# Optimization experiments

Hardware: AMD Instinct MI355X
Metric: run time of the kernel (lower is better)

## Reference

```python
import jax, jax.numpy as jnp
import numpy as np

B, L, H, N = 8, 2048, 512, 64  # batch, seq_len, d_model, SSM state size


def setup_inputs() -> dict:
    key = jax.random.key(0)
    ks = jax.random.split(key, 10)
    x = jax.random.normal(ks[0], (B, L, H), jnp.float32)
    # S4D-style parameters (diagonal SSM, S4D-Lin init)
    log_dt = jnp.log(1e-3) + jax.random.uniform(ks[1], (H,), jnp.float32) * (jnp.log(1e-1) - jnp.log(1e-3))
    A_re = -0.5 * jnp.ones((H, N), jnp.float32)
    A_im = jnp.tile(np.pi * jnp.arange(N, dtype=np.float32), (H, 1))
    C_re = jax.random.normal(ks[2], (H, N), jnp.float32) * (0.5 ** 0.5)
    C_im = jax.random.normal(ks[3], (H, N), jnp.float32) * (0.5 ** 0.5)
    D_skip = jax.random.normal(ks[4], (H,), jnp.float32)
    # S4 output linear (GLU): d_model -> 2*d_model, then gated
    W_out = jax.random.normal(ks[5], (2 * H, H), jnp.float32) / np.sqrt(H)
    b_out = jnp.zeros((2 * H,), jnp.float32)
    # LayerNorms
    g1 = jnp.ones((H,), jnp.float32); beta1 = jnp.zeros((H,), jnp.float32)
    g2 = jnp.ones((H,), jnp.float32); beta2 = jnp.zeros((H,), jnp.float32)
    # 1x1 conv FFN (kernel_size=1 => pointwise linear), d_ff = d_model
    W1 = jax.random.normal(ks[6], (H, H), jnp.float32) / np.sqrt(H)
    bc1 = jnp.zeros((H,), jnp.float32)
    W2 = jax.random.normal(ks[7], (H, H), jnp.float32) / np.sqrt(H)
    bc2 = jnp.zeros((H,), jnp.float32)
    return dict(x=x, log_dt=log_dt, A_re=A_re, A_im=A_im, C_re=C_re, C_im=C_im,
                D_skip=D_skip, W_out=W_out, b_out=b_out, g1=g1, beta1=beta1,
                g2=g2, beta2=beta2, W1=W1, bc1=bc1, W2=W2, bc2=bc2)


def _layer_norm(x, g, b):
    mu = jnp.mean(x, axis=-1, keepdims=True)
    var = jnp.mean((x - mu) ** 2, axis=-1, keepdims=True)
    return (x - mu) / jnp.sqrt(var + 1e-5) * g + b


def _s4(x, log_dt, A_re, A_im, C_re, C_im, D_skip, W_out, b_out):
    # x: (B, L, H) channels-last (transposed=False)
    Lx = x.shape[1]
    dt = jnp.exp(log_dt)                       # (H,)
    A = A_re + 1j * A_im                       # (H, N) diagonal state matrix
    dtA = A * dt[:, None]
    # ZOH discretization of C: Ct = C * (exp(dt*A) - 1) / A
    Ct = (C_re + 1j * C_im) * ((jnp.exp(dtA) - 1.0) / A)
    # Vandermonde kernel: K[h, l] = 2 Re sum_n Ct[h,n] exp(dt*A[h,n]*l)
    l = jnp.arange(Lx, dtype=jnp.float32)
    K = 2.0 * jnp.real(jnp.einsum('hn,hnl->hl', Ct, jnp.exp(dtA[:, :, None] * l)))
    # FFT long convolution (linear conv via zero-padded circular conv)
    u = jnp.swapaxes(x, 1, 2)                  # (B, H, L)
    n = 2 * Lx
    y = jnp.fft.irfft(jnp.fft.rfft(u, n) * jnp.fft.rfft(K, n)[None], n)[..., :Lx]
    y = y + D_skip[None, :, None] * u          # skip connection D*u
    y = jax.nn.gelu(y)                         # S4 default activation
    # output linear + GLU (S4 default postact)
    z = jnp.einsum('bhl,fh->bfl', y, W_out) + b_out[None, :, None]
    a, g = jnp.split(z, 2, axis=1)
    y = a * jax.nn.sigmoid(g)
    return jnp.swapaxes(y, 1, 2)               # (B, L, H)


def reference(x, log_dt, A_re, A_im, C_re, C_im, D_skip, W_out, b_out,
              g1, beta1, g2, beta2, W1, bc1, W2, bc2):
    new_x = _s4(x, log_dt, A_re, A_im, C_re, C_im, D_skip, W_out, b_out)
    x = x + new_x
    x = _layer_norm(x, g1, beta1)
    # FFN via 1x1 convs (pointwise linears); dropout is identity in eval
    y = jax.nn.relu(jnp.einsum('blh,fh->blf', x, W1) + bc1)
    y = jnp.einsum('blf,hf->blh', y, W2) + bc2
    return _layer_norm(x + y, g2, beta2)
```

## Files before the change

### kernel.cpp

```cpp
#include <hip/hip_runtime.h>
#include <cstddef>
#include <cstdint>

#define B_DIM 8
#define L_DIM 2048
#define H_DIM 512
#define N_DIM 64
#define HN (H_DIM * N_DIM)
#define BLH (B_DIM * L_DIM * H_DIM)
#define M_DIM (B_DIM * L_DIM)

typedef unsigned short u16;
typedef short bf16x8 __attribute__((ext_vector_type(8)));
typedef float floatx4 __attribute__((ext_vector_type(4)));

__device__ __forceinline__ float sigmoidf_(float v) {
    return 1.0f / (1.0f + __expf(-v));
}

__device__ __forceinline__ float gelu_tanh_(float x) {
    float x3 = x * x * x;
    float z = 0.7978845608028654f * fmaf(0.044715f, x3, x);
    float e = __expf(-2.0f * fabsf(z));
    float th = (1.0f - e) / (1.0f + e);
    th = copysignf(th, z);
    return 0.5f * x * (1.0f + th);
}

__device__ __forceinline__ u16 f2b(float f) {
    unsigned u = __float_as_uint(f);
    unsigned r = (u + 0x7fffu + ((u >> 16) & 1u)) >> 16;
    return (u16)r;
}
__device__ __forceinline__ float b2f(u16 u) {
    return __uint_as_float(((unsigned)u) << 16);
}
__device__ __forceinline__ void unpack2(unsigned u, float& a, float& b) {
    a = __uint_as_float(u << 16);
    b = __uint_as_float(u & 0xffff0000u);
}
__device__ __forceinline__ unsigned pack2(float a, float b) {
    return (unsigned)f2b(a) | ((unsigned)f2b(b) << 16);
}

__device__ __forceinline__ void csq(float& r, float& i) {
    float nr = r * r - i * i;
    i = 2.0f * r * i;
    r = nr;
}

__global__ __launch_bounds__(256) void cast3_kernel(
    const float* __restrict__ s0, const float* __restrict__ s1,
    const float* __restrict__ s2, u16* __restrict__ d0,
    u16* __restrict__ d1, u16* __restrict__ d2)
{
    int bid = blockIdx.x;
    const float* src; u16* dst; int off;
    if (bid < 512)      { src = s0; dst = d0; off = bid; }
    else if (bid < 768) { src = s1; dst = d1; off = bid - 512; }
    else                { src = s2; dst = d2; off = bid - 768; }
    int i = off * 256 + threadIdx.x;
    float4 v = *(const float4*)(src + (size_t)i * 4);
    uint2 p;
    p.x = pack2(v.x, v.y);
    p.y = pack2(v.z, v.w);
    *(uint2*)(dst + (size_t)i * 4) = p;
}

__global__ __launch_bounds__(256) void params_kernel(
    const float* __restrict__ log_dt, const float* __restrict__ A_re,
    const float* __restrict__ A_im, const float* __restrict__ C_re,
    const float* __restrict__ C_im, float* __restrict__ P,
    u16* __restrict__ Toep_bf)
{
    __shared__ float ktab_s[4][64];
    const int t = threadIdx.x;
    const int wv = t >> 6, lane = t & 63;
    const int i = blockIdx.x * 256 + t;
    const int h = i >> 6;

    float dt = expf(log_dt[h]);
    float Ar = A_re[i], Ai = A_im[i];
    float ar = dt * Ar, ai = dt * Ai;
    float e = expf(ar);
    float wr = e * cosf(ai);
    float wi = e * sinf(ai);
    float em1r = wr - 1.0f, em1i = wi;
    float inv = 1.0f / fmaf(Ar, Ar, Ai * Ai);
    float qr = fmaf(em1r, Ar, em1i * Ai) * inv;
    float qi = fmaf(em1i, Ar, -(em1r * Ai)) * inv;
    float Cr = C_re[i], Ci = C_im[i];
    float c2r = 2.0f * (Cr * qr - Ci * qi);
    float c2i = 2.0f * (Cr * qi + Ci * qr);
    P[i]          = wr;
    P[HN + i]     = wi;
    P[2 * HN + i] = c2r;
    P[3 * HN + i] = c2i;

    float pr = 1.0f, pi = 0.0f;
    for (int tau = 0; tau < 64; ++tau) {
        float term = c2r * pr - c2i * pi;
        #pragma unroll
        for (int m = 32; m > 0; m >>= 1) term += __shfl_xor(term, m, 64);
        if (lane == 0) ktab_s[wv][tau] = term;
        float nr = pr * wr - pi * wi, ni = pr * wi + pi * wr;
        pr = nr; pi = ni;
    }
    __syncthreads();

    const int h0 = blockIdx.x * 4;
    #pragma unroll
    for (int r = 0; r < 8; ++r) {
        int c = t + r * 256;
        int hh = c >> 9, rem = c & 511;
        int tt = rem >> 3, j0 = (rem & 7) * 8;
        u16 vv[8];
        #pragma unroll
        for (int jj = 0; jj < 8; ++jj) {
            int j = j0 + jj;
            vv[jj] = (j <= tt) ? f2b(ktab_s[hh][tt - j]) : (u16)0;
        }
        *(uint4*)&Toep_bf[((size_t)(h0 + hh) << 12) + (tt << 6) + j0] = *(uint4*)vv;
    }
}

__global__ __launch_bounds__(256) void xtrans_kernel(
    const float* __restrict__ x, u16* __restrict__ XT)
{
    __shared__ float tile[32][33];
    int b  = blockIdx.z;
    int l0 = blockIdx.x * 32;
    int h0 = blockIdx.y * 32;
    int tx = threadIdx.x & 31;
    int ty = threadIdx.x >> 5;
    #pragma unroll
    for (int r = 0; r < 4; ++r)
        tile[ty + r * 8][tx] = x[((size_t)b * L_DIM + l0 + ty + r * 8) * H_DIM + h0 + tx];
    __syncthreads();
    #pragma unroll
    for (int r = 0; r < 4; ++r)
        XT[((size_t)b * H_DIM + h0 + ty + r * 8) * L_DIM + l0 + tx] = f2b(tile[tx][ty + r * 8]);
}

__global__ __launch_bounds__(256) void ssm_chunk_kernel(
    const u16* __restrict__ XT, const float* __restrict__ P,
    const u16* __restrict__ Toep_bf, const float* __restrict__ D_skip,
    u16* __restrict__ YT)
{
    __shared__ u16 U[128 * 72];
    __shared__ u16 S[128 * 136];
    __shared__ u16 EVT[13312];
    u16* E  = EVT;
    u16* Tp = EVT;
    u16* V  = EVT + 4608;

    const int h    = blockIdx.x;
    const int b0   = blockIdx.y * 4;
    const int t    = threadIdx.x;
    const int lane = t & 63;
    const int wv   = t >> 6;
    const int lm   = lane & 15, lq = lane >> 4;

    const int pidx = (h << 6) + lane;
    const float wr  = P[pidx],          wi  = P[HN + pidx];
    const float c2r = P[2 * HN + pidx], c2i = P[3 * HN + pidx];

    #pragma unroll
    for (int r = 0; r < 4; ++r) {
        int idx = t + r * 256;
        int row = idx >> 3, ch = idx & 7;
        const u16* gp = XT + (((size_t)(b0 + (row >> 5)) * H_DIM + h) << 11)
                           + ((row & 31) << 6) + (ch << 3);
        *(uint4*)&U[row * 72 + ch * 8] = *(const uint4*)gp;
    }

    float bwr, bwi;
    {
        float g16r = wr, g16i = wi;
        csq(g16r, g16i); csq(g16r, g16i); csq(g16r, g16i); csq(g16r, g16i);
        if (wv == 0)      { bwr = 1.0f; bwi = 0.0f; }
        else if (wv == 1) { bwr = g16r; bwi = g16i; }
        else if (wv == 2) { bwr = g16r; bwi = g16i; csq(bwr, bwi); }
        else {
            float g32r = g16r, g32i = g16i; csq(g32r, g32i);
            bwr = g32r * g16r - g32i * g16i;
            bwi = g32r * g16i + g32i * g16r;
        }
    }

    {
        float pr = bwr, pi = bwi;
        #pragma unroll
        for (int jk = 0; jk < 16; ++jk) {
            int k = (wv << 4) + jk;
            int j = 63 - k;
            E[(2 * lane) * 72 + j]     = f2b(pr);
            E[(2 * lane + 1) * 72 + j] = f2b(pi);
            float nr = pr * wr - pi * wi, ni = pr * wi + pi * wr;
            pr = nr; pi = ni;
        }
    }
    __syncthreads();

    {
        const int wm = wv >> 1, wn = wv & 1;
        floatx4 acc[4][4] = {};
        #pragma unroll
        for (int ks = 0; ks < 2; ++ks) {
            bf16x8 af[4], bfv[4];
            #pragma unroll
            for (int i = 0; i < 4; ++i)
                af[i] = *(const bf16x8*)&E[(wm * 64 + i * 16 + lm) * 72 + ks * 32 + lq * 8];
            #pragma unroll
            for (int j = 0; j < 4; ++j)
                bfv[j] = *(const bf16x8*)&U[(wn * 64 + j * 16 + lm) * 72 + ks * 32 + lq * 8];
            #pragma unroll
            for (int i = 0; i < 4; ++i) {
                #pragma unroll
                for (int j = 0; j < 4; ++j)
                    acc[i][j] = __builtin_amdgcn_mfma_f32_16x16x32_bf16(af[i], bfv[j], acc[i][j], 0, 0, 0);
            }
        }
        #pragma unroll
        for (int i = 0; i < 4; ++i) {
            #pragma unroll
            for (int j = 0; j < 4; ++j) {
                int ncol = wn * 64 + j * 16 + lm;
                int m0   = wm * 64 + i * 16 + lq * 4;
                u16 pk[4];
                #pragma unroll
                for (int r = 0; r < 4; ++r) pk[r] = f2b(acc[i][j][r]);
                *(uint2*)&S[ncol * 136 + m0] = *(uint2*)pk;
            }
        }
    }
    __syncthreads();

    {
        float pr = bwr, pi = bwi;
        {
            float nr = pr * wr - pi * wi, ni = pr * wi + pi * wr;
            pr = nr; pi = ni;
        }
        #pragma unroll
        for (int jk = 1; jk <= 16; ++jk) {
            int tr = (wv << 4) + jk - 1;
            float qr = c2r * pr - c2i * pi;
            float qi = c2r * pi + c2i * pr;
            V[tr * 136 + 2 * lane]     = f2b(qr);
            V[tr * 136 + 2 * lane + 1] = f2b(-qi);
            float nr = pr * wr - pi * wi, ni = pr * wi + pi * wr;
            pr = nr; pi = ni;
        }
        #pragma unroll
        for (int r = 0; r < 2; ++r) {
            int idx = t + r * 256;
            int row = idx >> 3, ch = idx & 7;
            *(uint4*)&Tp[row * 72 + ch * 8] =
                *(const uint4*)&Toep_bf[((size_t)h << 12) + (row << 6) + (ch << 3)];
        }
        float wTr = wr, wTi = wi;
        csq(wTr, wTi); csq(wTr, wTi); csq(wTr, wTi);
        csq(wTr, wTi); csq(wTr, wTi); csq(wTr, wTi);
        float Sr = 0.0f, Si = 0.0f;
        const int n2 = lane * 2;
        for (int c = 0; c < 32; ++c) {
            int base = (wv * 32 + c) * 136 + n2;
            unsigned lv = *(unsigned*)&S[base];
            float lr, li;
            unpack2(lv, lr, li);
            *(unsigned*)&S[base] = pack2(Sr, Si);
            float nSr = wTr * Sr - wTi * Si + lr;
            Si = wTr * Si + wTi * Sr + li;
            Sr = nSr;
        }
    }
    __syncthreads();

    {
        const float Dh = D_skip[h];
        floatx4 acc[4][2] = {};
        #pragma unroll
        for (int ks = 0; ks < 6; ++ks) {
            bf16x8 af[4], bfv[2];
            if (ks < 2) {
                #pragma unroll
                for (int i = 0; i < 4; ++i)
                    af[i] = *(const bf16x8*)&Tp[(i * 16 + lm) * 72 + ks * 32 + lq * 8];
                #pragma unroll
                for (int j = 0; j < 2; ++j)
                    bfv[j] = *(const bf16x8*)&U[(wv * 32 + j * 16 + lm) * 72 + ks * 32 + lq * 8];
            } else {
                #pragma unroll
                for (int i = 0; i < 4; ++i)
                    af[i] = *(const bf16x8*)&V[(i * 16 + lm) * 136 + (ks - 2) * 32 + lq * 8];
                #pragma unroll
                for (int j = 0; j < 2; ++j)
                    bfv[j] = *(const bf16x8*)&S[(wv * 32 + j * 16 + lm) * 136 + (ks - 2) * 32 + lq * 8];
            }
            #pragma unroll
            for (int i = 0; i < 4; ++i) {
                #pragma unroll
                for (int j = 0; j < 2; ++j)
                    acc[i][j] = __builtin_amdgcn_mfma_f32_16x16x32_bf16(af[i], bfv[j], acc[i][j], 0, 0, 0);
            }
        }
        #pragma unroll
        for (int j = 0; j < 2; ++j) {
            int ncol = wv * 32 + j * 16 + lm;
            int bloc = ncol >> 5, c = ncol & 31;
            size_t gbase = (((size_t)(b0 + bloc) * H_DIM + h) << 11) + (c << 6);
            #pragma unroll
            for (int i = 0; i < 4; ++i) {
                int t0 = i * 16 + lq * 4;
                u16 upk[4];
                *(uint2*)upk = *(const uint2*)&U[ncol * 72 + t0];
                u16 opk[4];
                #pragma unroll
                for (int r = 0; r < 4; ++r) {
                    float uvv = b2f(upk[r]);
                    float yv = gelu_tanh_(fmaf(Dh, uvv, acc[i][j][r]));
                    opk[r] = f2b(yv);
                }
                *(uint2*)&YT[gbase + t0] = *(uint2*)opk;
            }
        }
    }
}

__global__ __launch_bounds__(256) void ytrans_kernel(
    const u16* __restrict__ YT, u16* __restrict__ Y)
{
    __shared__ u16 tile[32][33];
    int b  = blockIdx.z;
    int l0 = blockIdx.x * 32;
    int h0 = blockIdx.y * 32;
    int tx = threadIdx.x & 31;
    int ty = threadIdx.x >> 5;
    #pragma unroll
    for (int r = 0; r < 4; ++r)
        tile[ty + r * 8][tx] = YT[((size_t)b * H_DIM + h0 + ty + r * 8) * L_DIM + l0 + tx];
    __syncthreads();
    #pragma unroll
    for (int r = 0; r < 4; ++r)
        Y[((size_t)b * L_DIM + l0 + ty + r * 8) * H_DIM + h0 + tx] = tile[tx][ty + r * 8];
}

__device__ __forceinline__ void stage_tile_512(
    const u16* __restrict__ g, u16* lds, int row0, int k0)
{
    const int t = threadIdx.x;
    const int row  = t >> 2;
    const int csrc = (t & 3) ^ ((t >> 3) & 3);
    const u16* gp = g + (size_t)(row0 + row) * 512 + k0 + csrc * 8;
    __builtin_amdgcn_global_load_lds(
        (const __attribute__((address_space(1))) unsigned int*)gp,
        (__attribute__((address_space(3))) unsigned int*)(lds + (size_t)t * 8),
        16, 0, 0);
}

__global__ __launch_bounds__(512) void gemm1_glu_kernel(
    const u16* __restrict__ A, const u16* __restrict__ Wo,
    const float* __restrict__ bo, const float* __restrict__ x,
    u16* __restrict__ out)
{
    __shared__ u16 As[2][128 * 32];
    __shared__ u16 Ba[2][128 * 32];
    __shared__ u16 Bg[2][128 * 32];
    const int t    = threadIdx.x;
    const int lane = t & 63;
    const int wv   = t >> 6;
    const int wm   = wv >> 2, wn = wv & 3;
    const int lm   = lane & 15, lq = lane >> 4;
    const int sw   = (lq ^ ((lm >> 1) & 3)) * 8;
    const int m0   = blockIdx.x * 128, n0 = blockIdx.y * 128;
    floatx4 accA[4][2] = {};
    floatx4 accG[4][2] = {};

    stage_tile_512(A, As[0], m0, 0);
    stage_tile_512(Wo, Ba[0], n0, 0);
    stage_tile_512(Wo, Bg[0], 512 + n0, 0);
    __syncthreads();

    int cur = 0;
    for (int k0 = 32; k0 < 512; k0 += 32) {
        const int nx = cur ^ 1;
        stage_tile_512(A, As[nx], m0, k0);
        stage_tile_512(Wo, Ba[nx], n0, k0);
        stage_tile_512(Wo, Bg[nx], 512 + n0, k0);

        bf16x8 af[4], ba[2], bg[2];
        #pragma unroll
        for (int i = 0; i < 4; ++i)
            af[i] = *(const bf16x8*)&As[cur][(wm * 64 + i * 16 + lm) * 32 + sw];
        #pragma unroll
        for (int j = 0; j < 2; ++j) {
            ba[j] = *(const bf16x8*)&Ba[cur][(wn * 32 + j * 16 + lm) * 32 + sw];
            bg[j] = *(const bf16x8*)&Bg[cur][(wn * 32 + j * 16 + lm) * 32 + sw];
        }
        #pragma unroll
        for (int i = 0; i < 4; ++i) {
            #pragma unroll
            for (int j = 0; j < 2; ++j) {
                accA[i][j] = __builtin_amdgcn_mfma_f32_16x16x32_bf16(af[i], ba[j], accA[i][j], 0, 0, 0);
                accG[i][j] = __builtin_amdgcn_mfma_f32_16x16x32_bf16(af[i], bg[j], accG[i][j], 0, 0, 0);
            }
        }
        __syncthreads();
        cur = nx;
    }
    {
        bf16x8 af[4], ba[2], bg[2];
        #pragma unroll
        for (int i = 0; i < 4; ++i)
            af[i] = *(const bf16x8*)&As[cur][(wm * 64 + i * 16 + lm) * 32 + sw];
        #pragma unroll
        for (int j = 0; j < 2; ++j) {
            ba[j] = *(const bf16x8*)&Ba[cur][(wn * 32 + j * 16 + lm) * 32 + sw];
            bg[j] = *(const bf16x8*)&Bg[cur][(wn * 32 + j * 16 + lm) * 32 + sw];
        }
        #pragma unroll
        for (int i = 0; i < 4; ++i) {
            #pragma unroll
            for (int j = 0; j < 2; ++j) {
                accA[i][j] = __builtin_amdgcn_mfma_f32_16x16x32_bf16(af[i], ba[j], accA[i][j], 0, 0, 0);
                accG[i][j] = __builtin_amdgcn_mfma_f32_16x16x32_bf16(af[i], bg[j], accG[i][j], 0, 0, 0);
            }
        }
    }
    #pragma unroll
    for (int j = 0; j < 2; ++j) {
        int n = n0 + wn * 32 + j * 16 + lm;
        float bav = bo[n], bgv = bo[512 + n];
        #pragma unroll
        for (int i = 0; i < 4; ++i) {
            #pragma unroll
            for (int r = 0; r < 4; ++r) {
                int m = m0 + wm * 64 + i * 16 + lq * 4 + r;
                float av = accA[i][j][r] + bav;
                float gv = accG[i][j][r] + bgv;
                float xv = x[(size_t)m * 512 + n];
                out[(size_t)m * 512 + n] = f2b(fmaf(av, sigmoidf_(gv), xv));
            }
        }
    }
}

__global__ __launch_bounds__(512) void gemm_relu_kernel(
    const u16* __restrict__ A, const u16* __restrict__ Bw,
    const float* __restrict__ bias, u16* __restrict__ C)
{
    __shared__ u16 As[2][128 * 32];
    __shared__ u16 Bs[2][128 * 32];
    const int t    = threadIdx.x;
    const int lane = t & 63;
    const int wv   = t >> 6;
    const int wm   = wv >> 2, wn = wv & 3;
    const int lm   = lane & 15, lq = lane >> 4;
    const int sw   = (lq ^ ((lm >> 1) & 3)) * 8;
    const int m0   = blockIdx.x * 128, n0 = blockIdx.y * 128;
    floatx4 acc[4][2] = {};

    stage_tile_512(A, As[0], m0, 0);
    stage_tile_512(Bw, Bs[0], n0, 0);
    __syncthreads();

    int cur = 0;
    for (int k0 = 32; k0 < 512; k0 += 32) {
        const int nx = cur ^ 1;
        stage_tile_512(A, As[nx], m0, k0);
        stage_tile_512(Bw, Bs[nx], n0, k0);

        bf16x8 af[4], bfr[2];
        #pragma unroll
        for (int i = 0; i < 4; ++i)
            af[i] = *(const bf16x8*)&As[cur][(wm * 64 + i * 16 + lm) * 32 + sw];
        #pragma unroll
        for (int j = 0; j < 2; ++j)
            bfr[j] = *(const bf16x8*)&Bs[cur][(wn * 32 + j * 16 + lm) * 32 + sw];
        #pragma unroll
        for (int i = 0; i < 4; ++i) {
            #pragma unroll
            for (int j = 0; j < 2; ++j)
                acc[i][j] = __builtin_amdgcn_mfma_f32_16x16x32_bf16(af[i], bfr[j], acc[i][j], 0, 0, 0);
        }
        __syncthreads();
        cur = nx;
    }
    {
        bf16x8 af[4], bfr[2];
        #pragma unroll
        for (int i = 0; i < 4; ++i)
            af[i] = *(const bf16x8*)&As[cur][(wm * 64 + i * 16 + lm) * 32 + sw];
        #pragma unroll
        for (int j = 0; j < 2; ++j)
            bfr[j] = *(const bf16x8*)&Bs[cur][(wn * 32 + j * 16 + lm) * 32 + sw];
        #pragma unroll
        for (int i = 0; i < 4; ++i) {
            #pragma unroll
            for (int j = 0; j < 2; ++j)
                acc[i][j] = __builtin_amdgcn_mfma_f32_16x16x32_bf16(af[i], bfr[j], acc[i][j], 0, 0, 0);
        }
    }
    #pragma unroll
    for (int j = 0; j < 2; ++j) {
        int n = n0 + wn * 32 + j * 16 + lm;
        float bv = bias[n];
        #pragma unroll
        for (int i = 0; i < 4; ++i) {
            #pragma unroll
            for (int r = 0; r < 4; ++r) {
                int m = m0 + wm * 64 + i * 16 + lq * 4 + r;
                float v = fmaxf(acc[i][j][r] + bv, 0.0f);
                C[(size_t)m * 512 + n] = f2b(v);
            }
        }
    }
}

__global__ __launch_bounds__(512) void gemm2_ln_kernel(
    const u16* __restrict__ A, const u16* __restrict__ Bw,
    const float* __restrict__ bias, const u16* __restrict__ res,
    const float* __restrict__ gamma, const float* __restrict__ beta,
    float* __restrict__ out)
{
    __shared__ u16 As[2][32 * 32];
    __shared__ u16 Bs[2][512 * 32];
    __shared__ float2 lnred[32 * 8];
    const int t    = threadIdx.x;
    const int lane = t & 63;
    const int wv   = t >> 6;
    const int lm   = lane & 15, lq = lane >> 4;
    const int sw   = (lq ^ ((lm >> 1) & 3)) * 8;
    const int m0   = blockIdx.x * 32;
    floatx4 acc[2][4] = {};

    const int csrc = (t & 3) ^ ((t >> 3) & 3);

    {
        #pragma unroll
        for (int r = 0; r < 4; ++r) {
            int row = (t >> 2) + r * 128;
            const u16* gp = Bw + (size_t)row * 512 + csrc * 8;
            __builtin_amdgcn_global_load_lds(
                (const __attribute__((address_space(1))) unsigned int*)gp,
                (__attribute__((address_space(3))) unsigned int*)(&Bs[0][0] + (size_t)t * 8 + (size_t)r * 4096),
                16, 0, 0);
        }
        if (t < 128) {
            int row = t >> 2;
            const u16* gp = A + (size_t)(m0 + row) * 512 + csrc * 8;
            __builtin_amdgcn_global_load_lds(
                (const __attribute__((address_space(1))) unsigned int*)gp,
                (__attribute__((address_space(3))) unsigned int*)(&As[0][0] + (size_t)t * 8),
                16, 0, 0);
        }
    }
    __syncthreads();

    int cur = 0;
    for (int k0 = 32; k0 < 512; k0 += 32) {
        const int nx = cur ^ 1;
        #pragma unroll
        for (int r = 0; r < 4; ++r) {
            int row = (t >> 2) + r * 128;
            const u16* gp = Bw + (size_t)row * 512 + k0 + csrc * 8;
            __builtin_amdgcn_global_load_lds(
                (const __attribute__((address_space(1))) unsigned int*)gp,
                (__attribute__((address_space(3))) unsigned int*)(&Bs[nx][0] + (size_t)t * 8 + (size_t)r * 4096),
                16, 0, 0);
        }
        if (t < 128) {
            int row = t >> 2;
            const u16* gp = A + (size_t)(m0 + row) * 512 + k0 + csrc * 8;
            __builtin_amdgcn_global_load_lds(
                (const __attribute__((address_space(1))) unsigned int*)gp,
                (__attribute__((address_space(3))) unsigned int*)(&As[nx][0] + (size_t)t * 8),
                16, 0, 0);
        }

        bf16x8 af[2], bfr[4];
        #pragma unroll
        for (int i = 0; i < 2; ++i)
            af[i] = *(const bf16x8*)&As[cur][(i * 16 + lm) * 32 + sw];
        #pragma unroll
        for (int j = 0; j < 4; ++j)
            bfr[j] = *(const bf16x8*)&Bs[cur][(wv * 64 + j * 16 + lm) * 32 + sw];
        #pragma unroll
        for (int i = 0; i < 2; ++i) {
            #pragma unroll
            for (int j = 0; j < 4; ++j)
                acc[i][j] = __builtin_amdgcn_mfma_f32_16x16x32_bf16(af[i], bfr[j], acc[i][j], 0, 0, 0);
        }
        __syncthreads();
        cur = nx;
    }
    {
        bf16x8 af[2], bfr[4];
        #pragma unroll
        for (int i = 0; i < 2; ++i)
            af[i] = *(const bf16x8*)&As[cur][(i * 16 + lm) * 32 + sw];
        #pragma unroll
        for (int j = 0; j < 4; ++j)
            bfr[j] = *(const bf16x8*)&Bs[cur][(wv * 64 + j * 16 + lm) * 32 + sw];
        #pragma unroll
        for (int i = 0; i < 2; ++i) {
            #pragma unroll
            for (int j = 0; j < 4; ++j)
                acc[i][j] = __builtin_amdgcn_mfma_f32_16x16x32_bf16(af[i], bfr[j], acc[i][j], 0, 0, 0);
        }
    }

    float bv[4], gv[4], btv[4];
    #pragma unroll
    for (int j = 0; j < 4; ++j) {
        int n = wv * 64 + j * 16 + lm;
        bv[j]  = bias[n];
        gv[j]  = gamma[n];
        btv[j] = beta[n];
    }
    #pragma unroll
    for (int i = 0; i < 2; ++i) {
        #pragma unroll
        for (int j = 0; j < 4; ++j) {
            int n = wv * 64 + j * 16 + lm;
            #pragma unroll
            for (int r = 0; r < 4; ++r) {
                int m = m0 + i * 16 + lq * 4 + r;
                acc[i][j][r] += bv[j] + b2f(res[(size_t)m * 512 + n]);
            }
        }
    }
    #pragma unroll
    for (int i = 0; i < 2; ++i) {
        #pragma unroll
        for (int r = 0; r < 4; ++r) {
            float s  = acc[i][0][r] + acc[i][1][r] + acc[i][2][r] + acc[i][3][r];
            float sq = acc[i][0][r] * acc[i][0][r] + acc[i][1][r] * acc[i][1][r]
                     + acc[i][2][r] * acc[i][2][r] + acc[i][3][r] * acc[i][3][r];
            #pragma unroll
            for (int msk = 1; msk < 16; msk <<= 1) {
                s  += __shfl_xor(s, msk, 64);
                sq += __shfl_xor(sq, msk, 64);
            }
            if (lm == 0) {
                float2 p; p.x = s; p.y = sq;
                lnred[(i * 16 + lq * 4 + r) * 8 + wv] = p;
            }
        }
    }
    __syncthreads();
    #pragma unroll
    for (int i = 0; i < 2; ++i) {
        #pragma unroll
        for (int r = 0; r < 4; ++r) {
            int row = i * 16 + lq * 4 + r;
            float s = 0.0f, sq = 0.0f;
            #pragma unroll
            for (int w = 0; w < 8; ++w) {
                float2 p = lnred[row * 8 + w];
                s += p.x; sq += p.y;
            }
            float mu  = s * (1.0f / 512.0f);
            float var = sq * (1.0f / 512.0f) - mu * mu;
            float rs  = rsqrtf(var + 1e-5f);
            #pragma unroll
            for (int j = 0; j < 4; ++j) {
                int n = wv * 64 + j * 16 + lm;
                out[(size_t)(m0 + row) * 512 + n] = fmaf((acc[i][j][r] - mu) * rs, gv[j], btv[j]);
            }
        }
    }
}

__global__ __launch_bounds__(256) void ln_bf_kernel(
    const u16* __restrict__ in,
    const float* __restrict__ gamma, const float* __restrict__ beta,
    u16* __restrict__ outb)
{
    int w    = threadIdx.x >> 6;
    int lane = threadIdx.x & 63;
    size_t row  = (size_t)blockIdx.x * 4 + w;
    size_t base = row * 512 + lane * 8;
    uint4 raw = *(const uint4*)(in + base);
    float v[8];
    unpack2(raw.x, v[0], v[1]); unpack2(raw.y, v[2], v[3]);
    unpack2(raw.z, v[4], v[5]); unpack2(raw.w, v[6], v[7]);
    float s = 0.0f, sq = 0.0f;
    #pragma unroll
    for (int i = 0; i < 8; ++i) { s += v[i]; sq = fmaf(v[i], v[i], sq); }
    #pragma unroll
    for (int m = 32; m > 0; m >>= 1) {
        s  += __shfl_xor(s, m, 64);
        sq += __shfl_xor(sq, m, 64);
    }
    float mu  = s * (1.0f / 512.0f);
    float var = sq * (1.0f / 512.0f) - mu * mu;
    float rs  = rsqrtf(var + 1e-5f);
    float g[8], bt[8];
    *(float4*)&g[0]  = *(const float4*)(gamma + lane * 8);
    *(float4*)&g[4]  = *(const float4*)(gamma + lane * 8 + 4);
    *(float4*)&bt[0] = *(const float4*)(beta + lane * 8);
    *(float4*)&bt[4] = *(const float4*)(beta + lane * 8 + 4);
    float o[8];
    #pragma unroll
    for (int i = 0; i < 8; ++i)
        o[i] = fmaf((v[i] - mu) * rs, g[i], bt[i]);
    uint4 p;
    p.x = pack2(o[0], o[1]); p.y = pack2(o[2], o[3]);
    p.z = pack2(o[4], o[5]); p.w = pack2(o[6], o[7]);
    *(uint4*)(outb + base) = p;
}

extern "C" void kernel_launch(void* const* d_in, const int* in_sizes, int n_in,
                              void* d_out, int out_size, void* d_ws, size_t ws_size,
                              hipStream_t stream)
{
    (void)in_sizes; (void)n_in; (void)out_size; (void)ws_size;
    const float* x      = (const float*)d_in[0];
    const float* log_dt = (const float*)d_in[1];
    const float* A_re   = (const float*)d_in[2];
    const float* A_im   = (const float*)d_in[3];
    const float* C_re   = (const float*)d_in[4];
    const float* C_im   = (const float*)d_in[5];
    const float* D_skip = (const float*)d_in[6];
    const float* W_out  = (const float*)d_in[7];
    const float* b_out  = (const float*)d_in[8];
    const float* g1     = (const float*)d_in[9];
    const float* beta1  = (const float*)d_in[10];
    const float* g2     = (const float*)d_in[11];
    const float* beta2  = (const float*)d_in[12];
    const float* W1     = (const float*)d_in[13];
    const float* bc1    = (const float*)d_in[14];
    const float* W2     = (const float*)d_in[15];
    const float* bc2    = (const float*)d_in[16];
    float* out = (float*)d_out;

    char*  wsb    = (char*)d_ws;
    float* P      = (float*)wsb;
    u16*   Toep   = (u16*)(wsb + 4 * HN * 4 + 512 * 64 * 4);
    u16*   Wobf   = Toep + 512 * 4096;
    u16*   W1bf   = Wobf + 1024 * 512;
    u16*   W2bf   = W1bf + 512 * 512;
    u16*   r1     = W2bf + 512 * 512;
    u16*   r2     = r1 + BLH;
    u16*   r3     = r2 + BLH;

    cast3_kernel<<<1024, 256, 0, stream>>>(W_out, W1, W2, Wobf, W1bf, W2bf);
    params_kernel<<<128, 256, 0, stream>>>(log_dt, A_re, A_im, C_re, C_im, P, Toep);
    xtrans_kernel<<<dim3(L_DIM / 32, H_DIM / 32, B_DIM), 256, 0, stream>>>(x, r1);
    ssm_chunk_kernel<<<dim3(H_DIM, 2), 256, 0, stream>>>(r1, P, Toep, D_skip, r2);
    ytrans_kernel<<<dim3(L_DIM / 32, H_DIM / 32, B_DIM), 256, 0, stream>>>(r2, r3);
    gemm1_glu_kernel<<<dim3(M_DIM / 128, 4), 512, 0, stream>>>(r3, Wobf, b_out, x, r2);
    ln_bf_kernel<<<M_DIM / 4, 256, 0, stream>>>(r2, g1, beta1, r1);
    gemm_relu_kernel<<<dim3(M_DIM / 128, 4), 512, 0, stream>>>(r1, W1bf, bc1, r3);
    gemm2_ln_kernel<<<M_DIM / 32, 512, 0, stream>>>(r3, W2bf, bc2, r1, g2, beta2, out);
}
```

Before: 245.1 us.

## Fold LayerNorm1 into GEMM epilogues, fuse y-transpose into GEMM1, merge setup kernels

Merges the weight casts, parameter/Toeplitz setup and x transpose into a single setup kernel. The y transpose is dropped: GEMM1 reads the transposed SSM output directly and transposes it while staging into LDS. The standalone LayerNorm1 is also removed. GEMM1 emits per-row partial sum and sum-of-squares, and GEMM-relu applies the normalization algebraically, using W1 pre-scaled by g1 plus precomputed W1·g1 and W1·beta1 vectors. The final kernel recomputes LN1 on the fly for its residual. This cuts launches and two full-tensor passes, at the cost of uncoalesced 8-element scattered LDS writes in GEMM1 and LN applied to bf16-quantized pre-norm activations.

Result: faster. 240.1 us (-2.0%).

```diff
diff --git a/kernel.cpp b/kernel.cpp
--- a/kernel.cpp
+++ b/kernel.cpp
@@ -49,97 +49,124 @@
     r = nr;
 }
 
-__global__ __launch_bounds__(256) void cast3_kernel(
-    const float* __restrict__ s0, const float* __restrict__ s1,
-    const float* __restrict__ s2, u16* __restrict__ d0,
-    u16* __restrict__ d1, u16* __restrict__ d2)
-{
-    int bid = blockIdx.x;
-    const float* src; u16* dst; int off;
-    if (bid < 512)      { src = s0; dst = d0; off = bid; }
-    else if (bid < 768) { src = s1; dst = d1; off = bid - 512; }
-    else                { src = s2; dst = d2; off = bid - 768; }
-    int i = off * 256 + threadIdx.x;
-    float4 v = *(const float4*)(src + (size_t)i * 4);
-    uint2 p;
-    p.x = pack2(v.x, v.y);
-    p.y = pack2(v.z, v.w);
-    *(uint2*)(dst + (size_t)i * 4) = p;
-}
-
-__global__ __launch_bounds__(256) void params_kernel(
+__global__ __launch_bounds__(256) void setup_kernel(
+    const float* __restrict__ x, const float* __restrict__ W_out,
+    const float* __restrict__ W1, const float* __restrict__ W2,
     const float* __restrict__ log_dt, const float* __restrict__ A_re,
     const float* __restrict__ A_im, const float* __restrict__ C_re,
-    const float* __restrict__ C_im, float* __restrict__ P,
-    u16* __restrict__ Toep_bf)
-{
-    __shared__ float ktab_s[4][64];
-    const int t = threadIdx.x;
-    const int wv = t >> 6, lane = t & 63;
-    const int i = blockIdx.x * 256 + t;
-    const int h = i >> 6;
-
-    float dt = expf(log_dt[h]);
-    float Ar = A_re[i], Ai = A_im[i];
-    float ar = dt * Ar, ai = dt * Ai;
-    float e = expf(ar);
-    float wr = e * cosf(ai);
-    float wi = e * sinf(ai);
-    float em1r = wr - 1.0f, em1i = wi;
-    float inv = 1.0f / fmaf(Ar, Ar, Ai * Ai);
-    float qr = fmaf(em1r, Ar, em1i * Ai) * inv;
-    float qi = fmaf(em1i, Ar, -(em1r * Ai)) * inv;
-    float Cr = C_re[i], Ci = C_im[i];
-    float c2r = 2.0f * (Cr * qr - Ci * qi);
-    float c2i = 2.0f * (Cr * qi + Ci * qr);
-    P[i]          = wr;
-    P[HN + i]     = wi;
-    P[2 * HN + i] = c2r;
-    P[3 * HN + i] = c2i;
-
-    float pr = 1.0f, pi = 0.0f;
-    for (int tau = 0; tau < 64; ++tau) {
-        float term = c2r * pr - c2i * pi;
-        #pragma unroll
-        for (int m = 32; m > 0; m >>= 1) term += __shfl_xor(term, m, 64);
-        if (lane == 0) ktab_s[wv][tau] = term;
-        float nr = pr * wr - pi * wi, ni = pr * wi + pi * wr;
-        pr = nr; pi = ni;
-    }
-    __syncthreads();
-
-    const int h0 = blockIdx.x * 4;
-    #pragma unroll
-    for (int r = 0; r < 8; ++r) {
-        int c = t + r * 256;
-        int hh = c >> 9, rem = c & 511;
-        int tt = rem >> 3, j0 = (rem & 7) * 8;
-        u16 vv[8];
-        #pragma unroll
-        for (int jj = 0; jj < 8; ++jj) {
-            int j = j0 + jj;
-            vv[jj] = (j <= tt) ? f2b(ktab_s[hh][tt - j]) : (u16)0;
-        }
-        *(uint4*)&Toep_bf[((size_t)(h0 + hh) << 12) + (tt << 6) + j0] = *(uint4*)vv;
-    }
-}
-
-__global__ __launch_bounds__(256) void xtrans_kernel(
-    const float* __restrict__ x, u16* __restrict__ XT)
+    const float* __restrict__ C_im, const float* __restrict__ g1,
+    const float* __restrict__ beta1,
+    u16* __restrict__ XT, u16* __restrict__ Wobf, u16* __restrict__ W1gbf,
+    u16* __restrict__ W2bf, float* __restrict__ P, u16* __restrict__ Toep_bf,
+    float* __restrict__ c1, float* __restrict__ c2)
 {
     __shared__ float tile[32][33];
-    int b  = blockIdx.z;
-    int l0 = blockIdx.x * 32;
-    int h0 = blockIdx.y * 32;
-    int tx = threadIdx.x & 31;
-    int ty = threadIdx.x >> 5;
-    #pragma unroll
-    for (int r = 0; r < 4; ++r)
-        tile[ty + r * 8][tx] = x[((size_t)b * L_DIM + l0 + ty + r * 8) * H_DIM + h0 + tx];
-    __syncthreads();
-    #pragma unroll
-    for (int r = 0; r < 4; ++r)
-        XT[((size_t)b * H_DIM + h0 + ty + r * 8) * L_DIM + l0 + tx] = f2b(tile[tx][ty + r * 8]);
+    __shared__ float ktab_s[4][64];
+    const int bid = blockIdx.x;
+    const int t   = threadIdx.x;
+
+    if (bid < 8192) {
+        int b  = bid >> 10;
+        int hy = (bid >> 6) & 15;
+        int lx = bid & 63;
+        int l0 = lx * 32, h0 = hy * 32;
+        int tx = t & 31, ty = t >> 5;
+        #pragma unroll
+        for (int r = 0; r < 4; ++r)
+            tile[ty + r * 8][tx] = x[((size_t)b * L_DIM + l0 + ty + r * 8) * H_DIM + h0 + tx];
+        __syncthreads();
+        #pragma unroll
+        for (int r = 0; r < 4; ++r)
+            XT[(((size_t)b * H_DIM + h0 + ty + r * 8) << 11) + l0 + tx] = f2b(tile[tx][ty + r * 8]);
+    } else if (bid < 9216) {
+        int off = bid - 8192;
+        if (off < 512) {
+            int i = off * 256 + t;
+            float4 v = *(const float4*)(W_out + (size_t)i * 4);
+            uint2 p; p.x = pack2(v.x, v.y); p.y = pack2(v.z, v.w);
+            *(uint2*)(Wobf + (size_t)i * 4) = p;
+        } else if (off < 768) {
+            int i = (off - 512) * 256 + t;
+            float4 v = *(const float4*)(W1 + (size_t)i * 4);
+            int n = (i * 4) & 511;
+            float4 g = *(const float4*)(g1 + n);
+            uint2 p; p.x = pack2(v.x * g.x, v.y * g.y);
+            p.y = pack2(v.z * g.z, v.w * g.w);
+            *(uint2*)(W1gbf + (size_t)i * 4) = p;
+        } else {
+            int i = (off - 768) * 256 + t;
+            float4 v = *(const float4*)(W2 + (size_t)i * 4);
+            uint2 p; p.x = pack2(v.x, v.y); p.y = pack2(v.z, v.w);
+            *(uint2*)(W2bf + (size_t)i * 4) = p;
+        }
+    } else if (bid < 9344) {
+        const int wv = t >> 6, lane = t & 63;
+        const int i = (bid - 9216) * 256 + t;
+        const int h = i >> 6;
+        float dt = expf(log_dt[h]);
+        float Ar = A_re[i], Ai = A_im[i];
+        float ar = dt * Ar, ai = dt * Ai;
+        float e = expf(ar);
+        float wr = e * cosf(ai);
+        float wi = e * sinf(ai);
+        float em1r = wr - 1.0f, em1i = wi;
+        float inv = 1.0f / fmaf(Ar, Ar, Ai * Ai);
+        float qr = fmaf(em1r, Ar, em1i * Ai) * inv;
+        float qi = fmaf(em1i, Ar, -(em1r * Ai)) * inv;
+        float Cr = C_re[i], Ci = C_im[i];
+        float c2r = 2.0f * (Cr * qr - Ci * qi);
+        float c2i = 2.0f * (Cr * qi + Ci * qr);
+        P[i]          = wr;
+        P[HN + i]     = wi;
+        P[2 * HN + i] = c2r;
+        P[3 * HN + i] = c2i;
+
+        float pr = 1.0f, pi = 0.0f;
+        for (int tau = 0; tau < 64; ++tau) {
+            float term = c2r * pr - c2i * pi;
+            #pragma unroll
+            for (int m = 32; m > 0; m >>= 1) term += __shfl_xor(term, m, 64);
+            if (lane == 0) ktab_s[wv][tau] = term;
+            float nr = pr * wr - pi * wi, ni = pr * wi + pi * wr;
+            pr = nr; pi = ni;
+        }
+        __syncthreads();
+
+        const int h0 = (bid - 9216) * 4;
+        #pragma unroll
+        for (int r = 0; r < 8; ++r) {
+            int c = t + r * 256;
+            int hh = c >> 9, rem = c & 511;
+            int tt = rem >> 3, j0 = (rem & 7) * 8;
+            u16 vv[8];
+            #pragma unroll
+            for (int jj = 0; jj < 8; ++jj) {
+                int j = j0 + jj;
+                vv[jj] = (j <= tt) ? f2b(ktab_s[hh][tt - j]) : (u16)0;
+            }
+            *(uint4*)&Toep_bf[((size_t)(h0 + hh) << 12) + (tt << 6) + j0] = *(uint4*)vv;
+        }
+    } else {
+        int f = (bid - 9344) * 4 + (t >> 6);
+        int lane = t & 63;
+        int n = lane * 8;
+        float4 w0 = *(const float4*)(W1 + (size_t)f * 512 + n);
+        float4 w1v = *(const float4*)(W1 + (size_t)f * 512 + n + 4);
+        float4 ga = *(const float4*)(g1 + n);
+        float4 gb = *(const float4*)(g1 + n + 4);
+        float4 b0 = *(const float4*)(beta1 + n);
+        float4 b1 = *(const float4*)(beta1 + n + 4);
+        float s1 = w0.x * ga.x + w0.y * ga.y + w0.z * ga.z + w0.w * ga.w
+                 + w1v.x * gb.x + w1v.y * gb.y + w1v.z * gb.z + w1v.w * gb.w;
+        float s2 = w0.x * b0.x + w0.y * b0.y + w0.z * b0.z + w0.w * b0.w
+                 + w1v.x * b1.x + w1v.y * b1.y + w1v.z * b1.z + w1v.w * b1.w;
+        #pragma unroll
+        for (int m = 32; m > 0; m >>= 1) {
+            s1 += __shfl_xor(s1, m, 64);
+            s2 += __shfl_xor(s2, m, 64);
+        }
+        if (lane == 0) { c1[f] = s1; c2[f] = s2; }
+    }
 }
 
 __global__ __launch_bounds__(256) void ssm_chunk_kernel(
@@ -328,24 +355,6 @@
     }
 }
 
-__global__ __launch_bounds__(256) void ytrans_kernel(
-    const u16* __restrict__ YT, u16* __restrict__ Y)
-{
-    __shared__ u16 tile[32][33];
-    int b  = blockIdx.z;
-    int l0 = blockIdx.x * 32;
-    int h0 = blockIdx.y * 32;
-    int tx = threadIdx.x & 31;
-    int ty = threadIdx.x >> 5;
-    #pragma unroll
-    for (int r = 0; r < 4; ++r)
-        tile[ty + r * 8][tx] = YT[((size_t)b * H_DIM + h0 + ty + r * 8) * L_DIM + l0 + tx];
-    __syncthreads();
-    #pragma unroll
-    for (int r = 0; r < 4; ++r)
-        Y[((size_t)b * L_DIM + l0 + ty + r * 8) * H_DIM + h0 + tx] = tile[tx][ty + r * 8];
-}
-
 __device__ __forceinline__ void stage_tile_512(
     const u16* __restrict__ g, u16* lds, int row0, int k0)
 {
@@ -359,14 +368,32 @@
         16, 0, 0);
 }
 
+__device__ __forceinline__ uint4 ldA_yt(
+    const u16* __restrict__ YT, int b, int l0, int k0)
+{
+    const int k  = threadIdx.x >> 4;
+    const int lc = threadIdx.x & 15;
+    return *(const uint4*)(YT + (((size_t)(b * 512 + k0 + k)) << 11) + l0 + lc * 8);
+}
+__device__ __forceinline__ void dswA(u16* lds, uint4 av)
+{
+    const int k  = threadIdx.x >> 4;
+    const int lc = threadIdx.x & 15;
+    u16* p = lds + (lc * 8) * 32 + (((k >> 3) ^ (lc & 3)) << 3) + (k & 7);
+    const u16* s = (const u16*)&av;
+    #pragma unroll
+    for (int j = 0; j < 8; ++j) p[j * 32] = s[j];
+}
+
 __global__ __launch_bounds__(512) void gemm1_glu_kernel(
-    const u16* __restrict__ A, const u16* __restrict__ Wo,
+    const u16* __restrict__ YT, const u16* __restrict__ Wo,
     const float* __restrict__ bo, const float* __restrict__ x,
-    u16* __restrict__ out)
+    u16* __restrict__ out, float2* __restrict__ Pstats)
 {
     __shared__ u16 As[2][128 * 32];
     __shared__ u16 Ba[2][128 * 32];
     __shared__ u16 Bg[2][128 * 32];
+    __shared__ float2 red1[128][4];
     const int t    = threadIdx.x;
     const int lane = t & 63;
     const int wv   = t >> 6;
@@ -374,25 +401,33 @@
     const int lm   = lane & 15, lq = lane >> 4;
     const int sw   = (lq ^ ((lm >> 1) & 3)) * 8;
     const int m0   = blockIdx.x * 128, n0 = blockIdx.y * 128;
+    const int b    = m0 >> 11;
+    const int l0   = m0 & 2047;
     floatx4 accA[4][2] = {};
     floatx4 accG[4][2] = {};
 
-    stage_tile_512(A, As[0], m0, 0);
+    int swA[4];
+    #pragma unroll
+    for (int i = 0; i < 4; ++i)
+        swA[i] = (lq ^ ((i * 2 + (lm >> 3)) & 3)) * 8;
+
+    uint4 av = ldA_yt(YT, b, l0, 0);
     stage_tile_512(Wo, Ba[0], n0, 0);
     stage_tile_512(Wo, Bg[0], 512 + n0, 0);
+    dswA(As[0], av);
     __syncthreads();
 
     int cur = 0;
     for (int k0 = 32; k0 < 512; k0 += 32) {
         const int nx = cur ^ 1;
-        stage_tile_512(A, As[nx], m0, k0);
+        uint4 avn = ldA_yt(YT, b, l0, k0);
         stage_tile_512(Wo, Ba[nx], n0, k0);
         stage_tile_512(Wo, Bg[nx], 512 + n0, k0);
 
         bf16x8 af[4], ba[2], bg[2];
         #pragma unroll
         for (int i = 0; i < 4; ++i)
-            af[i] = *(const bf16x8*)&As[cur][(wm * 64 + i * 16 + lm) * 32 + sw];
+            af[i] = *(const bf16x8*)&As[cur][(wm * 64 + i * 16 + lm) * 32 + swA[i]];
         #pragma unroll
         for (int j = 0; j < 2; ++j) {
             ba[j] = *(const bf16x8*)&Ba[cur][(wn * 32 + j * 16 + lm) * 32 + sw];
@@ -406,6 +441,7 @@
                 accG[i][j] = __builtin_amdgcn_mfma_f32_16x16x32_bf16(af[i], bg[j], accG[i][j], 0, 0, 0);
             }
         }
+        dswA(As[nx], avn);
         __syncthreads();
         cur = nx;
     }
@@ -413,7 +449,7 @@
         bf16x8 af[4], ba[2], bg[2];
         #pragma unroll
         for (int i = 0; i < 4; ++i)
-            af[i] = *(const bf16x8*)&As[cur][(wm * 64 + i * 16 + lm) * 32 + sw];
+            af[i] = *(const bf16x8*)&As[cur][(wm * 64 + i * 16 + lm) * 32 + swA[i]];
         #pragma unroll
         for (int j = 0; j < 2; ++j) {
             ba[j] = *(const bf16x8*)&Ba[cur][(wn * 32 + j * 16 + lm) * 32 + sw];
@@ -428,30 +464,57 @@
             }
         }
     }
+
+    float bav[2], bgv[2];
     #pragma unroll
     for (int j = 0; j < 2; ++j) {
         int n = n0 + wn * 32 + j * 16 + lm;
-        float bav = bo[n], bgv = bo[512 + n];
-        #pragma unroll
-        for (int i = 0; i < 4; ++i) {
-            #pragma unroll
-            for (int r = 0; r < 4; ++r) {
-                int m = m0 + wm * 64 + i * 16 + lq * 4 + r;
-                float av = accA[i][j][r] + bav;
-                float gv = accG[i][j][r] + bgv;
+        bav[j] = bo[n]; bgv[j] = bo[512 + n];
+    }
+    #pragma unroll
+    for (int i = 0; i < 4; ++i) {
+        #pragma unroll
+        for (int r = 0; r < 4; ++r) {
+            int row = wm * 64 + i * 16 + lq * 4 + r;
+            int m = m0 + row;
+            float s = 0.0f, sq = 0.0f;
+            #pragma unroll
+            for (int j = 0; j < 2; ++j) {
+                int n = n0 + wn * 32 + j * 16 + lm;
+                float a_ = accA[i][j][r] + bav[j];
+                float g_ = accG[i][j][r] + bgv[j];
                 float xv = x[(size_t)m * 512 + n];
-                out[(size_t)m * 512 + n] = f2b(fmaf(av, sigmoidf_(gv), xv));
-            }
-        }
+                float ov = fmaf(a_, sigmoidf_(g_), xv);
+                out[(size_t)m * 512 + n] = f2b(ov);
+                s += ov; sq = fmaf(ov, ov, sq);
+            }
+            #pragma unroll
+            for (int msk = 1; msk < 16; msk <<= 1) {
+                s  += __shfl_xor(s, msk, 64);
+                sq += __shfl_xor(sq, msk, 64);
+            }
+            if (lm == 0) { float2 p; p.x = s; p.y = sq; red1[row][wn] = p; }
+        }
+    }
+    __syncthreads();
+    if (t < 128) {
+        float s = 0.0f, sq = 0.0f;
+        #pragma unroll
+        for (int w = 0; w < 4; ++w) { float2 p = red1[t][w]; s += p.x; sq += p.y; }
+        float2 o; o.x = s; o.y = sq;
+        Pstats[(size_t)(m0 + t) * 4 + blockIdx.y] = o;
     }
 }
 
 __global__ __launch_bounds__(512) void gemm_relu_kernel(
     const u16* __restrict__ A, const u16* __restrict__ Bw,
-    const float* __restrict__ bias, u16* __restrict__ C)
+    const float* __restrict__ bias, const float2* __restrict__ Pstats,
+    const float* __restrict__ c1, const float* __restrict__ c2,
+    u16* __restrict__ C)
 {
     __shared__ u16 As[2][128 * 32];
     __shared__ u16 Bs[2][128 * 32];
+    __shared__ float musig[128][2];
     const int t    = threadIdx.x;
     const int lane = t & 63;
     const int wv   = t >> 6;
@@ -461,6 +524,18 @@
     const int m0   = blockIdx.x * 128, n0 = blockIdx.y * 128;
     floatx4 acc[4][2] = {};
 
+    if (t < 128) {
+        float s = 0.0f, sq = 0.0f;
+        #pragma unroll
+        for (int w = 0; w < 4; ++w) {
+            float2 p = Pstats[(size_t)(m0 + t) * 4 + w];
+            s += p.x; sq += p.y;
+        }
+        float mu  = s * (1.0f / 512.0f);
+        float var = sq * (1.0f / 512.0f) - mu * mu;
+        musig[t][0] = mu;
+        musig[t][1] = rsqrtf(var + 1e-5f);
+    }
     stage_tile_512(A, As[0], m0, 0);
     stage_tile_512(Bw, Bs[0], n0, 0);
     __syncthreads();
@@ -502,17 +577,25 @@
                 acc[i][j] = __builtin_amdgcn_mfma_f32_16x16x32_bf16(af[i], bfr[j], acc[i][j], 0, 0, 0);
         }
     }
+    float c1v[2], c2v[2];
     #pragma unroll
     for (int j = 0; j < 2; ++j) {
         int n = n0 + wn * 32 + j * 16 + lm;
-        float bv = bias[n];
-        #pragma unroll
-        for (int i = 0; i < 4; ++i) {
-            #pragma unroll
-            for (int r = 0; r < 4; ++r) {
-                int m = m0 + wm * 64 + i * 16 + lq * 4 + r;
-                float v = fmaxf(acc[i][j][r] + bv, 0.0f);
-                C[(size_t)m * 512 + n] = f2b(v);
+        c1v[j] = c1[n];
+        c2v[j] = c2[n] + bias[n];
+    }
+    #pragma unroll
+    for (int i = 0; i < 4; ++i) {
+        #pragma unroll
+        for (int r = 0; r < 4; ++r) {
+            int row = wm * 64 + i * 16 + lq * 4 + r;
+            float mu = musig[row][0], rs = musig[row][1];
+            float nmr = -rs * mu;
+            #pragma unroll
+            for (int j = 0; j < 2; ++j) {
+                int n = n0 + wn * 32 + j * 16 + lm;
+                float v = fmaf(rs, acc[i][j][r], fmaf(nmr, c1v[j], c2v[j]));
+                C[(size_t)(m0 + row) * 512 + n] = f2b(fmaxf(v, 0.0f));
             }
         }
     }
@@ -521,12 +604,15 @@
 __global__ __launch_bounds__(512) void gemm2_ln_kernel(
     const u16* __restrict__ A, const u16* __restrict__ Bw,
     const float* __restrict__ bias, const u16* __restrict__ res,
+    const float2* __restrict__ Pstats,
+    const float* __restrict__ g1, const float* __restrict__ beta1,
     const float* __restrict__ gamma, const float* __restrict__ beta,
     float* __restrict__ out)
 {
     __shared__ u16 As[2][32 * 32];
     __shared__ u16 Bs[2][512 * 32];
     __shared__ float2 lnred[32 * 8];
+    __shared__ float musig2[32][2];
     const int t    = threadIdx.x;
     const int lane = t & 63;
     const int wv   = t >> 6;
@@ -537,6 +623,18 @@
 
     const int csrc = (t & 3) ^ ((t >> 3) & 3);
 
+    if (t < 32) {
+        float s = 0.0f, sq = 0.0f;
+        #pragma unroll
+        for (int w = 0; w < 4; ++w) {
+            float2 p = Pstats[(size_t)(m0 + t) * 4 + w];
+            s += p.x; sq += p.y;
+        }
+        float mu  = s * (1.0f / 512.0f);
+        float var = sq * (1.0f / 512.0f) - mu * mu;
+        musig2[t][0] = mu;
+        musig2[t][1] = rsqrtf(var + 1e-5f);
+    }
     {
         #pragma unroll
         for (int r = 0; r < 4; ++r) {
@@ -611,23 +709,28 @@
         }
     }
 
-    float bv[4], gv[4], btv[4];
+    float bv[4], gv1[4], bt1[4], gv[4], btv[4];
     #pragma unroll
     for (int j = 0; j < 4; ++j) {
         int n = wv * 64 + j * 16 + lm;
         bv[j]  = bias[n];
+        gv1[j] = g1[n];
+        bt1[j] = beta1[n];
         gv[j]  = gamma[n];
         btv[j] = beta[n];
     }
     #pragma unroll
     for (int i = 0; i < 2; ++i) {
         #pragma unroll
-        for (int j = 0; j < 4; ++j) {
-            int n = wv * 64 + j * 16 + lm;
-            #pragma unroll
-            for (int r = 0; r < 4; ++r) {
-                int m = m0 + i * 16 + lq * 4 + r;
-                acc[i][j][r] += bv[j] + b2f(res[(size_t)m * 512 + n]);
+        for (int r = 0; r < 4; ++r) {
+            int row = i * 16 + lq * 4 + r;
+            float mu1 = musig2[row][0], rs1 = musig2[row][1];
+            int m = m0 + row;
+            #pragma unroll
+            for (int j = 0; j < 4; ++j) {
+                int n = wv * 64 + j * 16 + lm;
+                float zl = fmaf((b2f(res[(size_t)m * 512 + n]) - mu1) * rs1, gv1[j], bt1[j]);
+                acc[i][j][r] += bv[j] + zl;
             }
         }
     }
@@ -671,45 +774,6 @@
             }
         }
     }
-}
-
-__global__ __launch_bounds__(256) void ln_bf_kernel(
-    const u16* __restrict__ in,
-    const float* __restrict__ gamma, const float* __restrict__ beta,
-    u16* __restrict__ outb)
-{
-    int w    = threadIdx.x >> 6;
-    int lane = threadIdx.x & 63;
-    size_t row  = (size_t)blockIdx.x * 4 + w;
-    size_t base = row * 512 + lane * 8;
-    uint4 raw = *(const uint4*)(in + base);
-    float v[8];
-    unpack2(raw.x, v[0], v[1]); unpack2(raw.y, v[2], v[3]);
-    unpack2(raw.z, v[4], v[5]); unpack2(raw.w, v[6], v[7]);
-    float s = 0.0f, sq = 0.0f;
-    #pragma unroll
-    for (int i = 0; i < 8; ++i) { s += v[i]; sq = fmaf(v[i], v[i], sq); }
-    #pragma unroll
-    for (int m = 32; m > 0; m >>= 1) {
-        s  += __shfl_xor(s, m, 64);
-        sq += __shfl_xor(sq, m, 64);
-    }
-    float mu  = s * (1.0f / 512.0f);
-    float var = sq * (1.0f / 512.0f) - mu * mu;
-    float rs  = rsqrtf(var + 1e-5f);
-    float g[8], bt[8];
-    *(float4*)&g[0]  = *(const float4*)(gamma + lane * 8);
-    *(float4*)&g[4]  = *(const float4*)(gamma + lane * 8 + 4);
-    *(float4*)&bt[0] = *(const float4*)(beta + lane * 8);
-    *(float4*)&bt[4] = *(const float4*)(beta + lane * 8 + 4);
-    float o[8];
-    #pragma unroll
-    for (int i = 0; i < 8; ++i)
-        o[i] = fmaf((v[i] - mu) * rs, g[i], bt[i]);
-    uint4 p;
-    p.x = pack2(o[0], o[1]); p.y = pack2(o[2], o[3]);
-    p.z = pack2(o[4], o[5]); p.w = pack2(o[6], o[7]);
-    *(uint4*)(outb + base) = p;
 }
 
 extern "C" void kernel_launch(void* const* d_in, const int* in_sizes, int n_in,
@@ -736,23 +800,24 @@
     const float* bc2    = (const float*)d_in[16];
     float* out = (float*)d_out;
 
-    char*  wsb    = (char*)d_ws;
-    float* P      = (float*)wsb;
-    u16*   Toep   = (u16*)(wsb + 4 * HN * 4 + 512 * 64 * 4);
-    u16*   Wobf   = Toep + 512 * 4096;
-    u16*   W1bf   = Wobf + 1024 * 512;
-    u16*   W2bf   = W1bf + 512 * 512;
-    u16*   r1     = W2bf + 512 * 512;
-    u16*   r2     = r1 + BLH;
-    u16*   r3     = r2 + BLH;
-
-    cast3_kernel<<<1024, 256, 0, stream>>>(W_out, W1, W2, Wobf, W1bf, W2bf);
-    params_kernel<<<128, 256, 0, stream>>>(log_dt, A_re, A_im, C_re, C_im, P, Toep);
-    xtrans_kernel<<<dim3(L_DIM / 32, H_DIM / 32, B_DIM), 256, 0, stream>>>(x, r1);
+    char*   wsb    = (char*)d_ws;
+    float*  P      = (float*)wsb;
+    u16*    Toep   = (u16*)(wsb + 4 * HN * 4 + 512 * 64 * 4);
+    u16*    Wobf   = Toep + 512 * 4096;
+    u16*    W1bf   = Wobf + 1024 * 512;
+    u16*    W2bf   = W1bf + 512 * 512;
+    u16*    r1     = W2bf + 512 * 512;
+    u16*    r2     = r1 + BLH;
+    u16*    r3     = r2 + BLH;
+    float2* Pstats = (float2*)(r3 + BLH);
+    float*  c1     = (float*)(Pstats + (size_t)M_DIM * 4);
+    float*  c2     = c1 + 512;
+
+    setup_kernel<<<9472, 256, 0, stream>>>(x, W_out, W1, W2, log_dt, A_re, A_im,
+                                           C_re, C_im, g1, beta1,
+                                           r1, Wobf, W1bf, W2bf, P, Toep, c1, c2);
     ssm_chunk_kernel<<<dim3(H_DIM, 2), 256, 0, stream>>>(r1, P, Toep, D_skip, r2);
-    ytrans_kernel<<<dim3(L_DIM / 32, H_DIM / 32, B_DIM), 256, 0, stream>>>(r2, r3);
-    gemm1_glu_kernel<<<dim3(M_DIM / 128, 4), 512, 0, stream>>>(r3, Wobf, b_out, x, r2);
-    ln_bf_kernel<<<M_DIM / 4, 256, 0, stream>>>(r2, g1, beta1, r1);
-    gemm_relu_kernel<<<dim3(M_DIM / 128, 4), 512, 0, stream>>>(r1, W1bf, bc1, r3);
-    gemm2_ln_kernel<<<M_DIM / 32, 512, 0, stream>>>(r3, W2bf, bc2, r1, g2, beta2, out);
-}
+    gemm1_glu_kernel<<<dim3(M_DIM / 128, 4), 512, 0, stream>>>(r2, Wobf, b_out, x, r3, Pstats);
+    gemm_relu_kernel<<<dim3(M_DIM / 128, 4), 512, 0, stream>>>(r3, W1bf, bc1, Pstats, c1, c2, r1);
+    gemm2_ln_kernel<<<M_DIM / 32, 512, 0, stream>>>(r1, W2bf, bc2, r3, Pstats, g1, beta1, g2, beta2, out);
+}
```
